# Kernel optimization log

Measured on AMD Instinct MI355X. Metric: run time of the kernel, lower is better.

The kernel has to match this reference:

```python
import jax, jax.numpy as jnp
import numpy as np

DIM = 256        # data dimension D
NUM_ATOMS = 512  # codebook size K
N_COLS = 65536   # number of signal columns (batch*H*W flattened)


def setup_inputs() -> dict:
    key = jax.random.key(0)
    k1, k2 = jax.random.split(key)
    z_e = jax.random.normal(k1, (DIM, N_COLS), dtype=jnp.float32)
    # learned parameter: nn.Parameter(torch.randn(num_atoms, dim))
    dictionary = jax.random.normal(k2, (NUM_ATOMS, DIM), dtype=jnp.float32)
    return {"z_e": z_e, "dictionary": dictionary}


def reference(z_e, dictionary):
    """Faithful JAX version of DictionaryLearningOMP.forward.

    The torch loop recomputes sparse_code = pinv(D) @ X on EVERY iteration
    (it never restricts to the selected atoms I), so sparse_code is constant
    across iterations: at iteration 2 the reconstruction distance between
    cur and last sparse codes is exactly 0 < epsilon and the loop stops.
    The argmax atom indices I are never used in the returned value, so the
    forward output is exactly (pinv(D) @ X).T.
    """
    D = dictionary.T                      # [dim, K]
    X = z_e.reshape(D.shape[0], -1)       # [dim, N]
    Dpinv = jnp.linalg.pinv(D)            # [K, dim]
    sparse_code = Dpinv @ X               # [K, N]
    return sparse_code.T                  # [N, K]
```

## Files before the change

### kernel.cpp

```cpp
#include <hip/hip_runtime.h>

typedef short  s16x8 __attribute__((ext_vector_type(8)));
typedef float  f32x4 __attribute__((ext_vector_type(4)));

#define NCOL 65536
#define DIMV 256
#define KATOMS 512

#define LAM_LO 25.0f
#define LAM_HI 1650.0f
#define C0 (2.0f / (LAM_LO + LAM_HI))

static __device__ __forceinline__ unsigned short f2bf(float x) {
  unsigned u = __float_as_uint(x);
  u += 0x7fffu + ((u >> 16) & 1u);
  return (unsigned short)(u >> 16);
}

__global__ __launch_bounds__(1024) void gram_init(const float* __restrict__ dict,
                                                  float* __restrict__ G,
                                                  float* __restrict__ X) {
  __shared__ float S0[KATOMS];
  __shared__ float Pp[4][DIMV];
  const int tid = threadIdx.x;
  const int r = blockIdx.x;
  if (tid < KATOMS) S0[tid] = dict[(size_t)tid * DIMV + r];
  __syncthreads();
  const int c = tid & 255, ks = tid >> 8;
  {
    float acc = 0.f;
    const int k0 = ks * 128;
#pragma unroll 8
    for (int k = 0; k < 128; ++k)
      acc += S0[k0 + k] * dict[(size_t)(k0 + k) * DIMV + c];
    Pp[ks][c] = acc;
  }
  __syncthreads();
  if (tid < 256) {
    const float g = ((Pp[0][c] + Pp[1][c]) + Pp[2][c]) + Pp[3][c];
    G[(size_t)r * DIMV + c] = g;
    X[(size_t)r * DIMV + c] = (r == c ? 2.f * C0 : 0.f) - C0 * C0 * g;
  }
}

__global__ __launch_bounds__(1024) void ns_iter(const float* __restrict__ G,
                                                const float* __restrict__ Xin,
                                                float* __restrict__ Xout,
                                                float a, float b) {
  __shared__ float S1[DIMV], Ps[DIMV];
  __shared__ float Pp[4][DIMV];
  const int tid = threadIdx.x;
  const int r = blockIdx.x;
  if (tid < 256) S1[tid] = Xin[(size_t)r * DIMV + tid];
  __syncthreads();
  const int c = tid & 255, ks = tid >> 8;
  const int k0 = ks * 64;
  {
    float p = 0.f;
#pragma unroll 8
    for (int k = 0; k < 64; ++k)
      p += S1[k0 + k] * G[(size_t)(k0 + k) * DIMV + c];
    Pp[ks][c] = p;
  }
  __syncthreads();
  if (tid < 256) Ps[c] = ((Pp[0][c] + Pp[1][c]) + Pp[2][c]) + Pp[3][c];
  __syncthreads();
  {
    float q = 0.f;
#pragma unroll 8
    for (int k = 0; k < 64; ++k)
      q += Ps[k0 + k] * Xin[(size_t)(k0 + k) * DIMV + c];
    Pp[ks][c] = q;
  }
  __syncthreads();
  if (tid < 256) {
    const float q = ((Pp[0][c] + Pp[1][c]) + Pp[2][c]) + Pp[3][c];
    Xout[(size_t)r * DIMV + c] = a * S1[c] - b * q;
  }
}

__global__ __launch_bounds__(1024) void make_m(const float* __restrict__ dict,
                                               const float* __restrict__ X,
                                               unsigned short* __restrict__ Mb) {
  __shared__ float S1[DIMV], S2[DIMV];
  __shared__ float Qp0[4][DIMV], Qp1[4][DIMV];
  const int tid = threadIdx.x;
  const int r = blockIdx.x;
  if (tid < 256) {
    S1[tid] = dict[(size_t)r * DIMV + tid];
    S2[tid] = dict[(size_t)(r + 256) * DIMV + tid];
  }
  __syncthreads();
  const int c = tid & 255, ks = tid >> 8;
  const int k0 = ks * 64;
  {
    float q0 = 0.f, q1 = 0.f;
#pragma unroll 8
    for (int k = 0; k < 64; ++k) {
      const float xv = X[(size_t)(k0 + k) * DIMV + c];
      q0 += S1[k0 + k] * xv;
      q1 += S2[k0 + k] * xv;
    }
    Qp0[ks][c] = q0;
    Qp1[ks][c] = q1;
  }
  __syncthreads();
  if (tid < 256) {
    const float q0 = ((Qp0[0][c] + Qp0[1][c]) + Qp0[2][c]) + Qp0[3][c];
    const float q1 = ((Qp1[0][c] + Qp1[1][c]) + Qp1[2][c]) + Qp1[3][c];
    Mb[(size_t)r * DIMV + c] = f2bf(q0);
    Mb[(size_t)(r + 256) * DIMV + c] = f2bf(q1);
  }
}

__global__ __launch_bounds__(512, 1) void big_gemm(const float* __restrict__ z,
                                                   const unsigned short* __restrict__ Mb,
                                                   float* __restrict__ out) {
  __shared__ unsigned int lds_w[64 * 132];
  const int tid = threadIdx.x;
  const int n0 = blockIdx.x * 64;

  {
    const int nq = tid & 15;
    const int dpb = tid >> 4;
#pragma unroll
    for (int i = 0; i < 4; ++i) {
      const int dp = i * 32 + dpb;
      const float* zp = z + (size_t)(2 * dp) * NCOL + n0 + 4 * nq;
      const f32x4 r0 = *(const f32x4*)zp;
      const f32x4 r1 = *(const f32x4*)(zp + NCOL);
#pragma unroll
      for (int j = 0; j < 4; ++j) {
        lds_w[(4 * nq + j) * 132 + dp] =
            (unsigned)f2bf(r0[j]) | ((unsigned)f2bf(r1[j]) << 16);
      }
    }
  }
  __syncthreads();

  const int l = tid & 63, w = tid >> 6;
  const int wn = w & 1, wk = w >> 1;
  const int mm = l & 15, q = l >> 4;
  const int nloc = wn * 32;
  const unsigned short* lds_s = (const unsigned short*)lds_w;

  f32x4 acc[2][8];
#pragma unroll
  for (int h = 0; h < 2; ++h)
#pragma unroll
    for (int s = 0; s < 8; ++s) acc[h][s] = (f32x4){0.f, 0.f, 0.f, 0.f};

#pragma unroll
  for (int step = 0; step < 8; ++step) {
    const int d0 = step * 32;
    s16x8 a0 = *(const s16x8*)(lds_s + (size_t)(nloc + mm) * 264 + d0 + 8 * q);
    s16x8 a1 = *(const s16x8*)(lds_s + (size_t)(nloc + mm + 16) * 264 + d0 + 8 * q);
    s16x8 b[8];
#pragma unroll
    for (int s = 0; s < 8; ++s) {
      const int k = wk * 128 + mm * 8 + s;
      b[s] = *(const s16x8*)(Mb + (size_t)k * DIMV + d0 + 8 * q);
    }
#pragma unroll
    for (int s = 0; s < 8; ++s) {
      acc[0][s] = __builtin_amdgcn_mfma_f32_16x16x32_bf16(a0, b[s], acc[0][s], 0, 0, 0);
      acc[1][s] = __builtin_amdgcn_mfma_f32_16x16x32_bf16(a1, b[s], acc[1][s], 0, 0, 0);
    }
  }

#pragma unroll
  for (int h = 0; h < 2; ++h)
#pragma unroll
    for (int r = 0; r < 4; ++r) {
      const int row = n0 + nloc + 16 * h + 4 * q + r;
      const int col0 = wk * 128 + mm * 8;
      f32x4 v0 = (f32x4){acc[h][0][r], acc[h][1][r], acc[h][2][r], acc[h][3][r]};
      f32x4 v1 = (f32x4){acc[h][4][r], acc[h][5][r], acc[h][6][r], acc[h][7][r]};
      float* op = out + (size_t)row * KATOMS + col0;
      *(f32x4*)op = v0;
      *(f32x4*)(op + 4) = v1;
    }
}

extern "C" void kernel_launch(void* const* d_in, const int* in_sizes, int n_in,
                              void* d_out, int out_size, void* d_ws, size_t ws_size,
                              hipStream_t stream) {
  const float* z    = (const float*)d_in[0];
  const float* dict = (const float*)d_in[1];
  float* out = (float*)d_out;

  const size_t MAT = (size_t)DIMV * DIMV;
  float* tail = out + (size_t)out_size - 3 * MAT;
  float* G  = tail;
  float* Xa = tail + MAT;
  float* Xb = tail + 2 * MAT;
  unsigned short* Mb = (unsigned short*)d_ws;

  gram_init<<<256, 1024, 0, stream>>>(dict, G, Xa);

  const double gammas[6] = {1.888912, 1.653116, 1.271098, 1.038134, 1.000731, 1.0};
  float* Xc = Xa;
  float* Xn = Xb;
  for (int it = 0; it < 6; ++it) {
    const float g = (float)gammas[it];
    ns_iter<<<256, 1024, 0, stream>>>(G, Xc, Xn, 2.f * g, g * g);
    float* tmp = Xc; Xc = Xn; Xn = tmp;
  }

  make_m<<<256, 1024, 0, stream>>>(dict, Xc, Mb);

  big_gemm<<<NCOL / 64, 512, 0, stream>>>(z, Mb, out);
}
```

Measured before the change: 288.4 us.

## Keep M fragments register-resident and process two column tiles per block

Result: faster. 255.8 us (-11.3%).

```diff
diff --git a/kernel.cpp b/kernel.cpp
--- a/kernel.cpp
+++ b/kernel.cpp
@@ -113,73 +113,74 @@
   }
 }
 
-__global__ __launch_bounds__(512, 1) void big_gemm(const float* __restrict__ z,
+__global__ __launch_bounds__(512, 2) void big_gemm(const float* __restrict__ z,
                                                    const unsigned short* __restrict__ Mb,
                                                    float* __restrict__ out) {
   __shared__ unsigned int lds_w[64 * 132];
   const int tid = threadIdx.x;
-  const int n0 = blockIdx.x * 64;
-
-  {
-    const int nq = tid & 15;
-    const int dpb = tid >> 4;
-#pragma unroll
-    for (int i = 0; i < 4; ++i) {
-      const int dp = i * 32 + dpb;
-      const float* zp = z + (size_t)(2 * dp) * NCOL + n0 + 4 * nq;
-      const f32x4 r0 = *(const f32x4*)zp;
-      const f32x4 r1 = *(const f32x4*)(zp + NCOL);
-#pragma unroll
-      for (int j = 0; j < 4; ++j) {
-        lds_w[(4 * nq + j) * 132 + dp] =
-            (unsigned)f2bf(r0[j]) | ((unsigned)f2bf(r1[j]) << 16);
+  const int l = tid & 63, w = tid >> 6;
+  const int mm = l & 15, q = l >> 4;
+  const unsigned short* lds_s = (const unsigned short*)lds_w;
+
+  s16x8 b[32];
+#pragma unroll
+  for (int dstep = 0; dstep < 8; ++dstep)
+#pragma unroll
+    for (int s = 0; s < 4; ++s)
+      b[dstep * 4 + s] = *(const s16x8*)(Mb + (size_t)(w * 64 + mm * 4 + s) * DIMV +
+                                         dstep * 32 + 8 * q);
+
+#pragma unroll 1
+  for (int t = 0; t < 2; ++t) {
+    const int n0 = blockIdx.x * 128 + t * 64;
+    __syncthreads();
+
+    {
+      const int nq = tid & 15, dpb = tid >> 4;
+#pragma unroll
+      for (int i = 0; i < 4; ++i) {
+        const int dp = i * 32 + dpb;
+        const float* zp = z + (size_t)(2 * dp) * NCOL + n0 + 4 * nq;
+        const f32x4 r0 = *(const f32x4*)zp;
+        const f32x4 r1 = *(const f32x4*)(zp + NCOL);
+#pragma unroll
+        for (int j = 0; j < 4; ++j)
+          lds_w[(4 * nq + j) * 132 + dp] =
+              (unsigned)f2bf(r0[j]) | ((unsigned)f2bf(r1[j]) << 16);
       }
     }
-  }
-  __syncthreads();
-
-  const int l = tid & 63, w = tid >> 6;
-  const int wn = w & 1, wk = w >> 1;
-  const int mm = l & 15, q = l >> 4;
-  const int nloc = wn * 32;
-  const unsigned short* lds_s = (const unsigned short*)lds_w;
-
-  f32x4 acc[2][8];
-#pragma unroll
-  for (int h = 0; h < 2; ++h)
-#pragma unroll
-    for (int s = 0; s < 8; ++s) acc[h][s] = (f32x4){0.f, 0.f, 0.f, 0.f};
-
-#pragma unroll
-  for (int step = 0; step < 8; ++step) {
-    const int d0 = step * 32;
-    s16x8 a0 = *(const s16x8*)(lds_s + (size_t)(nloc + mm) * 264 + d0 + 8 * q);
-    s16x8 a1 = *(const s16x8*)(lds_s + (size_t)(nloc + mm + 16) * 264 + d0 + 8 * q);
-    s16x8 b[8];
-#pragma unroll
-    for (int s = 0; s < 8; ++s) {
-      const int k = wk * 128 + mm * 8 + s;
-      b[s] = *(const s16x8*)(Mb + (size_t)k * DIMV + d0 + 8 * q);
+    __syncthreads();
+
+    f32x4 acc[4][4];
+#pragma unroll
+    for (int ns = 0; ns < 4; ++ns)
+#pragma unroll
+      for (int s = 0; s < 4; ++s) acc[ns][s] = (f32x4){0.f, 0.f, 0.f, 0.f};
+
+#pragma unroll
+    for (int dstep = 0; dstep < 8; ++dstep) {
+      s16x8 a[4];
+#pragma unroll
+      for (int ns = 0; ns < 4; ++ns)
+        a[ns] = *(const s16x8*)(lds_s + (size_t)(ns * 16 + mm) * 264 + dstep * 32 + 8 * q);
+#pragma unroll
+      for (int ns = 0; ns < 4; ++ns)
+#pragma unroll
+        for (int s = 0; s < 4; ++s)
+          acc[ns][s] = __builtin_amdgcn_mfma_f32_16x16x32_bf16(a[ns], b[dstep * 4 + s],
+                                                               acc[ns][s], 0, 0, 0);
     }
-#pragma unroll
-    for (int s = 0; s < 8; ++s) {
-      acc[0][s] = __builtin_amdgcn_mfma_f32_16x16x32_bf16(a0, b[s], acc[0][s], 0, 0, 0);
-      acc[1][s] = __builtin_amdgcn_mfma_f32_16x16x32_bf16(a1, b[s], acc[1][s], 0, 0, 0);
-    }
-  }
-
-#pragma unroll
-  for (int h = 0; h < 2; ++h)
-#pragma unroll
-    for (int r = 0; r < 4; ++r) {
-      const int row = n0 + nloc + 16 * h + 4 * q + r;
-      const int col0 = wk * 128 + mm * 8;
-      f32x4 v0 = (f32x4){acc[h][0][r], acc[h][1][r], acc[h][2][r], acc[h][3][r]};
-      f32x4 v1 = (f32x4){acc[h][4][r], acc[h][5][r], acc[h][6][r], acc[h][7][r]};
-      float* op = out + (size_t)row * KATOMS + col0;
-      *(f32x4*)op = v0;
-      *(f32x4*)(op + 4) = v1;
-    }
+
+#pragma unroll
+    for (int ns = 0; ns < 4; ++ns)
+#pragma unroll
+      for (int r = 0; r < 4; ++r) {
+        const int row = n0 + ns * 16 + 4 * q + r;
+        const int col0 = w * 64 + mm * 4;
+        f32x4 v = (f32x4){acc[ns][0][r], acc[ns][1][r], acc[ns][2][r], acc[ns][3][r]};
+        *(f32x4*)(out + (size_t)row * KATOMS + col0) = v;
+      }
+  }
 }
 
 extern "C" void kernel_launch(void* const* d_in, const int* in_sizes, int n_in,
@@ -209,5 +210,5 @@
 
   make_m<<<256, 1024, 0, stream>>>(dict, Xc, Mb);
 
-  big_gemm<<<NCOL / 64, 512, 0, stream>>>(z, Mb, out);
-}
+  big_gemm<<<NCOL / 128, 512, 0, stream>>>(z, Mb, out);
+}
```
